# Kernel optimization log

Measured on AMD Instinct MI355X. Metric: run time of the kernel, lower is better.

## Reference

```python
import jax, jax.numpy as jnp
import numpy as np

B, N_ATOM, N_TOK = 1, 1536, 384
C_ATOM, C_PAIR, C_TOK = 128, 16, 384
C_HID, H, L = 32, 4, 3
HID = 2 * C_ATOM  # n_transition = 2
N_QUERY, N_KEY, INF = 32, 128, 1e9


def _ln(x, gamma=None, beta=None, eps=1e-5):
    mu = jnp.mean(x, axis=-1, keepdims=True)
    var = jnp.mean(jnp.square(x - mu), axis=-1, keepdims=True)
    y = (x - mu) * jax.lax.rsqrt(var + eps)
    if gamma is not None:
        y = y * gamma
    if beta is not None:
        y = y + beta
    return y


def _adaln(a, s, gamma_s, Wg, bg, Ws):
    an = _ln(a)            # LN without affine
    sn = _ln(s, gamma_s)   # scale-only LN
    return jax.nn.sigmoid(sn @ Wg + bg) * an + sn @ Ws


def _block_mask():
    # AtomTransformer.forward: 32-query x 128-key block-local mask
    offset = N_QUERY // 2 - 0.5
    n_center = N_ATOM // N_QUERY + 1
    centers = offset + jnp.arange(n_center, dtype=jnp.float32) * N_QUERY
    idx = jnp.arange(N_ATOM, dtype=jnp.float32)[:, None]
    row = (jnp.abs(idx - centers[None, :]) < N_QUERY / 2).astype(jnp.float32)
    col = (jnp.abs(idx - centers[None, :]) < N_KEY / 2).astype(jnp.float32)
    return (row @ col.T - 1.0) * INF   # [N,N]: 0 in-window, -INF outside


def _forward(ref_pos, ref_mask, ref_element, ref_charge, ref_atom_name_chars,
             ref_space_uid, token_mask, atom_to_token_index,
             W_feats, W_ref_offset, W_inv_sq, W_valid, W_l, W_m,
             W_mlp1, W_mlp2, W_mlp3, W_out_tok,
             attn_ada_gamma_s, attn_ada_Wg, attn_ada_bg, attn_ada_Ws,
             Wq, bq, Wk, Wv, lnz_g, lnz_b, Wb, Wgate, Wo, Wsg, bsg,
             tr_ada_gamma_s, tr_ada_Wg, tr_ada_bg, tr_ada_Ws,
             tr_W1, tr_W2, tr_Wog, tr_bog, tr_Wout):
    # --- RefAtomFeatureEmbedder (AF3 Alg 5 lines 1-6) ---
    feats = jnp.concatenate([
        ref_pos, ref_mask[..., None], ref_element, ref_charge[..., None],
        ref_atom_name_chars.reshape(B, N_ATOM, -1), ref_space_uid[..., None]], axis=-1)
    cl = feats @ W_feats                                     # [B,N,C_ATOM]
    d = ref_pos[:, None, :, :] - ref_pos[:, :, None, :]      # d[l,m] = pos[m]-pos[l]
    v = (ref_space_uid[:, None, :] == ref_space_uid[:, :, None]).astype(jnp.float32)[..., None]
    plm = (d @ W_ref_offset) * v
    inv_sq = 1.0 / (1.0 + jnp.sum(d * d, axis=-1, keepdims=True))
    plm = plm + (inv_sq @ W_inv_sq) * v + (v @ W_valid) * v  # [B,N,N,C_PAIR]
    ql = cl
    # --- single -> pair conditioning + pair MLP ---
    crelu = jax.nn.relu(cl)
    plm = plm + (crelu @ W_l)[:, :, None, :] + (crelu @ W_m)[:, None, :, :]
    h = jax.nn.relu(plm) @ W_mlp1
    h = jax.nn.relu(h) @ W_mlp2
    h = jax.nn.relu(h) @ W_mlp3
    plm = plm + h
    # --- AtomTransformer (Alg 7) -> DiffusionTransformer (Alg 23) ---
    beta = _block_mask()                                     # [N,N]
    atom_mask = jnp.einsum('blt,bt->bl', atom_to_token_index, token_mask)
    mask_bias = (atom_mask - 1.0)[:, None, None, :] * INF    # [B,1,1,N]
    a, s = ql, cl
    inv_sqrt = 1.0 / np.sqrt(C_HID)
    for i in range(L):
        # AttentionPairBias (Alg 24)
        an = _adaln(a, s, attn_ada_gamma_s[i], attn_ada_Wg[i], attn_ada_bg[i], attn_ada_Ws[i])
        q = (an @ Wq[i] + bq[i]).reshape(B, N_ATOM, H, C_HID)
        k = (an @ Wk[i]).reshape(B, N_ATOM, H, C_HID)
        vv = (an @ Wv[i]).reshape(B, N_ATOM, H, C_HID)
        zb = _ln(plm, lnz_g[i], lnz_b[i]) @ Wb[i]            # [B,N,N,H]
        logits = (jnp.einsum('bqhc,bkhc->bhqk', q, k) * inv_sqrt
                  + jnp.moveaxis(zb, -1, 1) + beta[None, None] + mask_bias)
        A = jax.nn.softmax(logits, axis=-1)
        o = jnp.einsum('bhqk,bkhc->bqhc', A, vv)
        g = jax.nn.sigmoid(an @ Wgate[i]).reshape(B, N_ATOM, H, C_HID)
        o = (g * o).reshape(B, N_ATOM, H * C_HID) @ Wo[i]
        attn_out = jax.nn.sigmoid(s @ Wsg[i] + bsg[i]) * o
        # ConditionedTransitionBlock (Alg 25) on pre-attention a (Alg 23)
        tn = _adaln(a, s, tr_ada_gamma_s[i], tr_ada_Wg[i], tr_ada_bg[i], tr_ada_Ws[i])
        hh = jax.nn.silu(tn @ tr_W1[i]) * (tn @ tr_W2[i])
        tr_out = jax.nn.sigmoid(s @ tr_Wog[i] + tr_bog[i]) * (hh @ tr_Wout[i])
        a = attn_out + tr_out
    # --- mean-aggregate atoms -> tokens (Alg 5 line 15) ---
    al = jax.nn.relu(a @ W_out_tok)                          # [B,N,C_TOK]
    counts = jnp.maximum(jnp.sum(atom_to_token_index, axis=1), 1.0)
    a_tok = jnp.einsum('blt,blc->btc', atom_to_token_index, al) / counts[..., None]
    return a_tok


def setup_inputs() -> dict:
    key = jax.random.key(0)
    ks = iter(jax.random.split(key, 80))

    def nrm(shape, scale=0.02):
        return jax.random.normal(next(ks), shape, dtype=jnp.float32) * scale

    inp = {}
    inp['ref_pos'] = jax.random.normal(next(ks), (B, N_ATOM, 3), dtype=jnp.float32) * 3.0
    inp['ref_mask'] = jnp.ones((B, N_ATOM), jnp.float32)
    elem = jax.random.randint(next(ks), (B, N_ATOM), 0, 128)
    inp['ref_element'] = jax.nn.one_hot(elem, 128, dtype=jnp.float32)
    inp['ref_charge'] = jax.random.normal(next(ks), (B, N_ATOM), dtype=jnp.float32)
    chars = jax.random.randint(next(ks), (B, N_ATOM, 4), 0, 64)
    inp['ref_atom_name_chars'] = jax.nn.one_hot(chars, 64, dtype=jnp.float32)
    inp['ref_space_uid'] = jnp.broadcast_to(
        (jnp.arange(N_ATOM) // 8).astype(jnp.float32), (B, N_ATOM))
    inp['token_mask'] = jnp.ones((B, N_TOK), jnp.float32)
    tok = (jnp.arange(N_ATOM) * N_TOK) // N_ATOM  # ~4 atoms per token
    inp['atom_to_token_index'] = jnp.broadcast_to(
        jax.nn.one_hot(tok, N_TOK, dtype=jnp.float32), (B, N_ATOM, N_TOK))
    # embedder params
    inp['W_feats'] = nrm((390, C_ATOM))
    inp['W_ref_offset'] = nrm((3, C_PAIR))
    inp['W_inv_sq'] = nrm((1, C_PAIR))
    inp['W_valid'] = nrm((1, C_PAIR))
    inp['W_l'] = nrm((C_ATOM, C_PAIR))
    inp['W_m'] = nrm((C_ATOM, C_PAIR))
    inp['W_mlp1'] = nrm((C_PAIR, C_PAIR))
    inp['W_mlp2'] = nrm((C_PAIR, C_PAIR))
    inp['W_mlp3'] = nrm((C_PAIR, C_PAIR))
    inp['W_out_tok'] = nrm((C_ATOM, C_TOK))
    # DiffusionTransformer params, stacked over L blocks
    inp['attn_ada_gamma_s'] = jnp.ones((L, C_ATOM), jnp.float32)
    inp['attn_ada_Wg'] = nrm((L, C_ATOM, C_ATOM))
    inp['attn_ada_bg'] = jnp.zeros((L, C_ATOM), jnp.float32)
    inp['attn_ada_Ws'] = nrm((L, C_ATOM, C_ATOM))
    inp['Wq'] = nrm((L, C_ATOM, H * C_HID))
    inp['bq'] = jnp.zeros((L, H * C_HID), jnp.float32)
    inp['Wk'] = nrm((L, C_ATOM, H * C_HID))
    inp['Wv'] = nrm((L, C_ATOM, H * C_HID))
    inp['lnz_g'] = jnp.ones((L, C_PAIR), jnp.float32)
    inp['lnz_b'] = jnp.zeros((L, C_PAIR), jnp.float32)
    inp['Wb'] = nrm((L, C_PAIR, H))
    inp['Wgate'] = nrm((L, C_ATOM, H * C_HID))
    inp['Wo'] = nrm((L, H * C_HID, C_ATOM))
    inp['Wsg'] = nrm((L, C_ATOM, C_ATOM))
    inp['bsg'] = jnp.full((L, C_ATOM), -2.0, jnp.float32)
    inp['tr_ada_gamma_s'] = jnp.ones((L, C_ATOM), jnp.float32)
    inp['tr_ada_Wg'] = nrm((L, C_ATOM, C_ATOM))
    inp['tr_ada_bg'] = jnp.zeros((L, C_ATOM), jnp.float32)
    inp['tr_ada_Ws'] = nrm((L, C_ATOM, C_ATOM))
    inp['tr_W1'] = nrm((L, C_ATOM, HID))
    inp['tr_W2'] = nrm((L, C_ATOM, HID))
    inp['tr_Wog'] = nrm((L, C_ATOM, C_ATOM))
    inp['tr_bog'] = jnp.full((L, C_ATOM), -2.0, jnp.float32)
    inp['tr_Wout'] = nrm((L, HID, C_ATOM))
    return inp


def reference(ref_pos, ref_mask, ref_element, ref_charge, ref_atom_name_chars,
              ref_space_uid, token_mask, atom_to_token_index,
              W_feats, W_ref_offset, W_inv_sq, W_valid, W_l, W_m,
              W_mlp1, W_mlp2, W_mlp3, W_out_tok,
              attn_ada_gamma_s, attn_ada_Wg, attn_ada_bg, attn_ada_Ws,
              Wq, bq, Wk, Wv, lnz_g, lnz_b, Wb, Wgate, Wo, Wsg, bsg,
              tr_ada_gamma_s, tr_ada_Wg, tr_ada_bg, tr_ada_Ws,
              tr_W1, tr_W2, tr_Wog, tr_bog, tr_Wout):
    return _forward(ref_pos, ref_mask, ref_element, ref_charge, ref_atom_name_chars,
                    ref_space_uid, token_mask, atom_to_token_index,
                    W_feats, W_ref_offset, W_inv_sq, W_valid, W_l, W_m,
                    W_mlp1, W_mlp2, W_mlp3, W_out_tok,
                    attn_ada_gamma_s, attn_ada_Wg, attn_ada_bg, attn_ada_Ws,
                    Wq, bq, Wk, Wv, lnz_g, lnz_b, Wb, Wgate, Wo, Wsg, bsg,
                    tr_ada_gamma_s, tr_ada_Wg, tr_ada_bg, tr_ada_Ws,
                    tr_W1, tr_W2, tr_Wog, tr_bog, tr_Wout)
```

## Files before the change

kernel.cpp:

```cpp
#include <hip/hip_runtime.h>
#include <math.h>

#define N_ATOM 1536
#define NLAYER 3
#define NC     196608L
#define ZSTRIDE 786432L

struct GD { const float* A; const float* B; float* C; const float* ks; const float* bias;
            const float* sg; const float* ad; int act; int ldb; int ldc; int mode; };
struct GB { GD g[18]; };

__global__ __launch_bounds__(128) void embed_tok_kernel(
    const float* __restrict__ pos, const float* __restrict__ rmask,
    const float* __restrict__ elem, const float* __restrict__ charge,
    const float* __restrict__ chars, const float* __restrict__ uid,
    const float* __restrict__ Wf, const float* __restrict__ W_l, const float* __restrict__ W_m,
    const float* __restrict__ a2t, const float* __restrict__ tmask,
    float* __restrict__ cl, float* __restrict__ aa,
    float* __restrict__ pl, float* __restrict__ pm,
    int* __restrict__ tok, float* __restrict__ amask)
{
  int l = blockIdx.x, c = threadIdx.x;
  __shared__ int sidx[6];
  __shared__ float crow[128];
  if (elem[(long)l * 128 + c] > 0.5f) sidx[0] = c;
  float v0 = chars[(long)l * 256 + c];
  if (v0 > 0.5f) sidx[1 + (c >> 6)] = c & 63;
  float v1 = chars[(long)l * 256 + 128 + c];
  if (v1 > 0.5f) sidx[3 + (c >> 6)] = c & 63;
  for (int j = c; j < 384; j += 128)
    if (a2t[(long)l * 384 + j] > 0.5f) sidx[5] = j;
  __syncthreads();
  float acc = pos[l * 3 + 0] * Wf[c]
            + pos[l * 3 + 1] * Wf[128 + c]
            + pos[l * 3 + 2] * Wf[256 + c]
            + rmask[l] * Wf[384 + c]
            + Wf[(4 + sidx[0]) * 128 + c]
            + charge[l] * Wf[132 * 128 + c]
            + Wf[(133 + sidx[1]) * 128 + c]
            + Wf[(197 + sidx[2]) * 128 + c]
            + Wf[(261 + sidx[3]) * 128 + c]
            + Wf[(325 + sidx[4]) * 128 + c]
            + uid[l] * Wf[389 * 128 + c];
  long gi = (long)l * 128 + c;
  cl[gi] = acc; aa[gi] = acc; crow[c] = fmaxf(acc, 0.f);
  __syncthreads();
  if (c < 32) {
    const float* W = (c < 16) ? W_l : W_m;
    int o = c & 15;
    float s = 0.f;
    for (int cc = 0; cc < 128; cc++) s = fmaf(crow[cc], W[cc * 16 + o], s);
    if (c < 16) pl[l * 16 + o] = s; else pm[l * 16 + o] = s;
  }
  if (c == 127) {
    int j = sidx[5];
    tok[l] = j; amask[l] = tmask[j];
  }
}

__device__ __forceinline__ void gemm64_body(float* sm, const GD d, int row0, int col0) {
  float* As = sm; float* Bs = sm + 2176;
  float* rmu = sm + 4352;
  float* rsd = sm + 4416;
  int tid = threadIdx.x;
  if (d.mode >= 1) {
    int r = tid >> 2, sgi = tid & 3;
    const float* Ar = d.A + (long)(row0 + r) * 128 + sgi * 32;
    float4 vv[8];
    float s1 = 0.f;
#pragma unroll
    for (int c4 = 0; c4 < 8; c4++) {
      vv[c4] = *(const float4*)(Ar + c4 * 4);
      s1 += vv[c4].x + vv[c4].y + vv[c4].z + vv[c4].w;
    }
    s1 += __shfl_xor(s1, 1); s1 += __shfl_xor(s1, 2);
    float mu = s1 * (1.f / 128.f);
    float s2 = 0.f;
#pragma unroll
    for (int c4 = 0; c4 < 8; c4++) {
      float dx = vv[c4].x - mu, dy = vv[c4].y - mu, dz = vv[c4].z - mu, dw = vv[c4].w - mu;
      s2 += dx * dx + dy * dy + dz * dz + dw * dw;
    }
    s2 += __shfl_xor(s2, 1); s2 += __shfl_xor(s2, 2);
    if (sgi == 0) {
      rmu[r] = mu;
      rsd[r] = rsqrtf(s2 * (1.f / 128.f) + 1e-5f);
    }
  }
  int tx = tid & 15, ty = tid >> 4;
  float acc[4][4] = {};
  for (int k0 = 0; k0 < 128; k0 += 32) {
    __syncthreads();
    { int r = tid >> 3, k4 = tid & 7;
#pragma unroll
      for (int half = 0; half < 2; half++) {
        int row = r + half * 32;
        long gro = (long)(row0 + row) * 128 + k0 + k4 * 4;
        float4 v = *(const float4*)(d.A + gro);
        float vals[4] = {v.x, v.y, v.z, v.w};
        if (d.mode >= 1) {
          float mu = rmu[row], sd = rsd[row];
          if (d.mode == 2) {
            float4 sg4 = *(const float4*)(d.sg + gro);
            float4 ad4 = *(const float4*)(d.ad + gro);
            vals[0] = fmaf(sg4.x, (vals[0] - mu) * sd, ad4.x);
            vals[1] = fmaf(sg4.y, (vals[1] - mu) * sd, ad4.y);
            vals[2] = fmaf(sg4.z, (vals[2] - mu) * sd, ad4.z);
            vals[3] = fmaf(sg4.w, (vals[3] - mu) * sd, ad4.w);
          } else {
#pragma unroll
            for (int cc = 0; cc < 4; cc++) vals[cc] = (vals[cc] - mu) * sd;
          }
        }
        if (d.ks) {
          const float* kp = d.ks + k0 + k4 * 4;
#pragma unroll
          for (int cc = 0; cc < 4; cc++) vals[cc] *= kp[cc];
        }
        As[(k4 * 4 + 0) * 68 + row] = vals[0]; As[(k4 * 4 + 1) * 68 + row] = vals[1];
        As[(k4 * 4 + 2) * 68 + row] = vals[2]; As[(k4 * 4 + 3) * 68 + row] = vals[3];
      } }
    { int kk = tid >> 4, n4 = tid & 15;
#pragma unroll
      for (int half = 0; half < 2; half++) {
        int k = kk + half * 16;
        *(float4*)&Bs[k * 68 + n4 * 4] = *(const float4*)(d.B + (long)(k0 + k) * d.ldb + col0 + n4 * 4);
      } }
    __syncthreads();
#pragma unroll
    for (int kk = 0; kk < 32; kk++) {
      float4 a = *(const float4*)&As[kk * 68 + ty * 4];
      float4 b = *(const float4*)&Bs[kk * 68 + tx * 4];
      float av[4] = {a.x, a.y, a.z, a.w}, bv[4] = {b.x, b.y, b.z, b.w};
#pragma unroll
      for (int i = 0; i < 4; i++)
#pragma unroll
        for (int j = 0; j < 4; j++) acc[i][j] = fmaf(av[i], bv[j], acc[i][j]);
    }
  }
  __syncthreads();
#pragma unroll
  for (int i = 0; i < 4; i++) {
    int row = row0 + ty * 4 + i;
#pragma unroll
    for (int j = 0; j < 4; j++) {
      int col = col0 + tx * 4 + j;
      float x = acc[i][j];
      if (d.bias) x += d.bias[col];
      if (d.act == 1) x = 1.f / (1.f + expf(-x));
      else if (d.act == 2) x = fmaxf(x, 0.f);
      d.C[(long)row * d.ldc + col] = x;
    }
  }
}

__global__ __launch_bounds__(256) void gemm64(GB args)
{
  __shared__ float sm[4480];
  gemm64_body(sm, args.g[blockIdx.z], blockIdx.y * 64, blockIdx.x * 64);
}

__global__ __launch_bounds__(256) void zpre_kernel(
    const float* __restrict__ pos, const float* __restrict__ uid,
    const float* __restrict__ Wro, const float* __restrict__ Winv, const float* __restrict__ Wval,
    const float* __restrict__ M1, const float* __restrict__ M2, const float* __restrict__ M3,
    const float* __restrict__ Lg, const float* __restrict__ Lb, const float* __restrict__ Wb,
    const float* __restrict__ pl, const float* __restrict__ pm, float* __restrict__ zb,
    GB ba)
{
  __shared__ float sm[4480];
  int bid = blockIdx.x, tid = threadIdx.x;
  if (bid >= 768) {
    int u = bid - 768;
    GD d = ba.g[u / 48];
    int tt = u % 48;
    gemm64_body(sm, d, (tt >> 1) * 64, (tt & 1) * 64);
    return;
  }
  if (tid < 48)  sm[tid] = Wro[tid];
  if (tid < 16)  { sm[48 + tid] = Winv[tid]; sm[64 + tid] = Wval[tid]; }
  sm[80 + tid] = M1[tid]; sm[336 + tid] = M2[tid]; sm[592 + tid] = M3[tid];
  if (tid < 48)  { sm[848 + tid] = Lg[tid]; sm[896 + tid] = Lb[tid]; }
  if (tid < 192) sm[944 + tid] = Wb[tid];
  __syncthreads();
  const float* sWro = sm;      const float* sWinv = sm + 48;  const float* sWval = sm + 64;
  const float* sM1 = sm + 80;  const float* sM2 = sm + 336;   const float* sM3 = sm + 592;
  const float* sLg = sm + 848; const float* sLb = sm + 896;   const float* sWb = sm + 944;
  int b = bid >> 4;
  int pc = (bid & 15) * 256 + tid;
  int qi = pc >> 7, kj = pc & 127;
  int l = b * 32 + qi, m = b * 32 - 48 + kj;
  long base = (long)(b * 32 + qi) * 128 + kj;
  if (m < 0 || m >= N_ATOM) {
    for (int i = 0; i < NLAYER; i++)
      for (int h = 0; h < 4; h++) zb[i * ZSTRIDE + h * NC + base] = 0.f;
    return;
  }
  float dx = pos[m * 3 + 0] - pos[l * 3 + 0];
  float dy = pos[m * 3 + 1] - pos[l * 3 + 1];
  float dz = pos[m * 3 + 2] - pos[l * 3 + 2];
  float v = (uid[m] == uid[l]) ? 1.f : 0.f;
  float inv = 1.f / (1.f + dx * dx + dy * dy + dz * dz);
  float pv[16], ha[16], hb[16];
#pragma unroll
  for (int j = 0; j < 16; j++)
    pv[j] = v * (dx * sWro[j] + dy * sWro[16 + j] + dz * sWro[32 + j] + inv * sWinv[j] + sWval[j])
            + pl[l * 16 + j] + pm[m * 16 + j];
#pragma unroll
  for (int jo = 0; jo < 16; jo++) { float s = 0.f; for (int ji = 0; ji < 16; ji++) s = fmaf(fmaxf(pv[ji], 0.f), sM1[ji * 16 + jo], s); ha[jo] = s; }
#pragma unroll
  for (int jo = 0; jo < 16; jo++) { float s = 0.f; for (int ji = 0; ji < 16; ji++) s = fmaf(fmaxf(ha[ji], 0.f), sM2[ji * 16 + jo], s); hb[jo] = s; }
#pragma unroll
  for (int jo = 0; jo < 16; jo++) { float s = 0.f; for (int ji = 0; ji < 16; ji++) s = fmaf(fmaxf(hb[ji], 0.f), sM3[ji * 16 + jo], s); ha[jo] = s; }
#pragma unroll
  for (int j = 0; j < 16; j++) pv[j] += ha[j];
  for (int i = 0; i < NLAYER; i++) {
    float mu = 0.f;
#pragma unroll
    for (int j = 0; j < 16; j++) mu += pv[j];
    mu *= (1.f / 16.f);
    float var = 0.f;
#pragma unroll
    for (int j = 0; j < 16; j++) { float dd = pv[j] - mu; var += dd * dd; }
    var *= (1.f / 16.f);
    float rs = rsqrtf(var + 1e-5f);
    float zn[16];
#pragma unroll
    for (int j = 0; j < 16; j++) zn[j] = (pv[j] - mu) * rs * sLg[i * 16 + j] + sLb[i * 16 + j];
    for (int h = 0; h < 4; h++) {
      float s = 0.f;
#pragma unroll
      for (int j = 0; j < 16; j++) s = fmaf(zn[j], sWb[i * 64 + j * 4 + h], s);
      zb[i * ZSTRIDE + h * NC + base] = s;
    }
  }
}

__global__ __launch_bounds__(256) void attn_kernel(
    const float* __restrict__ qb, const float* __restrict__ kb, const float* __restrict__ vb,
    const float* __restrict__ gb, const float* __restrict__ zb, const float* __restrict__ amask,
    float* __restrict__ go)
{
  __shared__ float qs[16][36], ks[128][36], vs[128][36], ps[16][132];
  int bx = blockIdx.x, h = blockIdx.y, t = threadIdx.x;
  int b = bx >> 1, half = bx & 1;
  int q0 = b * 32 + half * 16;
  int kbase = b * 32 - 48;
  const float* zbh = zb + (long)h * NC;
  if (t < 128) {
    int qi = t >> 3, c4 = t & 7;
    *(float4*)&qs[qi][c4 * 4] = *(const float4*)(qb + (long)(q0 + qi) * 128 + h * 32 + c4 * 4);
  }
  for (int idx = t; idx < 128 * 8; idx += 256) {
    int kj = idx >> 3, c4 = idx & 7;
    int m = kbase + kj;
    float4 kv = make_float4(0.f, 0.f, 0.f, 0.f), vv = make_float4(0.f, 0.f, 0.f, 0.f);
    if (m >= 0 && m < N_ATOM) {
      kv = *(const float4*)(kb + (long)m * 128 + h * 32 + c4 * 4);
      vv = *(const float4*)(vb + (long)m * 128 + h * 32 + c4 * 4);
    }
    *(float4*)&ks[kj][c4 * 4] = kv;
    *(float4*)&vs[kj][c4 * 4] = vv;
  }
  __syncthreads();
  const float isq = 0.17677669529663687f;
  for (int p = t; p < 2048; p += 256) {
    int qi = p >> 7, kj = p & 127;
    int m = kbase + kj;
    float s = 0.f;
#pragma unroll
    for (int c4 = 0; c4 < 8; c4++) {
      float4 a = *(const float4*)&qs[qi][c4 * 4];
      float4 k4 = *(const float4*)&ks[kj][c4 * 4];
      s = fmaf(a.x, k4.x, s); s = fmaf(a.y, k4.y, s);
      s = fmaf(a.z, k4.z, s); s = fmaf(a.w, k4.w, s);
    }
    float logit;
    if (m >= 0 && m < N_ATOM) {
      logit = s * isq + zbh[(long)(q0 + qi) * 128 + kj] + (amask[m] - 1.f) * 1e9f;
    } else {
      logit = -1e9f;
    }
    ps[qi][kj] = logit;
  }
  __syncthreads();
  {
    int row = t >> 4, ln = t & 15;
    float mx = -1e30f;
    for (int kj = ln; kj < 128; kj += 16) mx = fmaxf(mx, ps[row][kj]);
#pragma unroll
    for (int o = 8; o > 0; o >>= 1) mx = fmaxf(mx, __shfl_xor(mx, o));
    float sm = 0.f;
    for (int kj = ln; kj < 128; kj += 16) { float e = expf(ps[row][kj] - mx); ps[row][kj] = e; sm += e; }
#pragma unroll
    for (int o = 8; o > 0; o >>= 1) sm += __shfl_xor(sm, o);
    float r = 1.f / sm;
    for (int kj = ln; kj < 128; kj += 16) ps[row][kj] *= r;
  }
  __syncthreads();
  {
    int qi = t >> 4, seg = (t >> 3) & 1, c4 = t & 7;
    float4 acc = make_float4(0.f, 0.f, 0.f, 0.f);
    int kj0 = seg * 64;
#pragma unroll 4
    for (int kj = kj0; kj < kj0 + 64; kj++) {
      float p = ps[qi][kj];
      float4 v = *(const float4*)&vs[kj][c4 * 4];
      acc.x = fmaf(p, v.x, acc.x); acc.y = fmaf(p, v.y, acc.y);
      acc.z = fmaf(p, v.z, acc.z); acc.w = fmaf(p, v.w, acc.w);
    }
    acc.x += __shfl_xor(acc.x, 8);
    acc.y += __shfl_xor(acc.y, 8);
    acc.z += __shfl_xor(acc.z, 8);
    acc.w += __shfl_xor(acc.w, 8);
    if (seg == 0) {
      long gi = (long)(q0 + qi) * 128 + h * 32 + c4 * 4;
      float4 g = *(const float4*)(gb + gi);
      acc.x *= g.x; acc.y *= g.y; acc.z *= g.z; acc.w *= g.w;
      *(float4*)(go + gi) = acc;
    }
  }
}

__global__ __launch_bounds__(256) void gemm_dual32(
    const float* __restrict__ A1, const float* __restrict__ B1,
    const float* __restrict__ h1, const float* __restrict__ h2, const float* __restrict__ B2,
    const float* __restrict__ g1, const float* __restrict__ g2,
    float* __restrict__ C)
{
  __shared__ float As[32 * 36];
  __shared__ float Bs[32 * 68];
  const int N = 128;
  int t = threadIdx.x;
  int row0 = blockIdx.y * 32, col0 = blockIdx.x * 64;
  int tx = t & 15, ty = t >> 4;
  float acc1[2][4] = {}, acc2[2][4] = {};
  for (int k0 = 0; k0 < 128; k0 += 32) {
    __syncthreads();
    { int r = t >> 3, k4 = t & 7;
      float4 v = *(const float4*)(A1 + (long)(row0 + r) * 128 + k0 + k4 * 4);
      As[(k4 * 4 + 0) * 36 + r] = v.x; As[(k4 * 4 + 1) * 36 + r] = v.y;
      As[(k4 * 4 + 2) * 36 + r] = v.z; As[(k4 * 4 + 3) * 36 + r] = v.w;
    }
    for (int e = t; e < 512; e += 256) {
      int k = e >> 4, n4 = e & 15;
      *(float4*)&Bs[k * 68 + n4 * 4] = *(const float4*)(B1 + (long)(k0 + k) * N + col0 + n4 * 4);
    }
    __syncthreads();
#pragma unroll
    for (int kk = 0; kk < 32; kk++) {
      float a0 = As[kk * 36 + ty * 2], a1 = As[kk * 36 + ty * 2 + 1];
      float4 b = *(const float4*)&Bs[kk * 68 + tx * 4];
      float bv[4] = {b.x, b.y, b.z, b.w};
#pragma unroll
      for (int j = 0; j < 4; j++) {
        acc1[0][j] = fmaf(a0, bv[j], acc1[0][j]);
        acc1[1][j] = fmaf(a1, bv[j], acc1[1][j]);
      }
    }
  }
  for (int k0 = 0; k0 < 256; k0 += 32) {
    __syncthreads();
    { int r = t >> 3, k4 = t & 7;
      long o = (long)(row0 + r) * 256 + k0 + k4 * 4;
      float4 x = *(const float4*)(h1 + o);
      float4 y = *(const float4*)(h2 + o);
      As[(k4 * 4 + 0) * 36 + r] = (x.x / (1.f + expf(-x.x))) * y.x;
      As[(k4 * 4 + 1) * 36 + r] = (x.y / (1.f + expf(-x.y))) * y.y;
      As[(k4 * 4 + 2) * 36 + r] = (x.z / (1.f + expf(-x.z))) * y.z;
      As[(k4 * 4 + 3) * 36 + r] = (x.w / (1.f + expf(-x.w))) * y.w;
    }
    for (int e = t; e < 512; e += 256) {
      int k = e >> 4, n4 = e & 15;
      *(float4*)&Bs[k * 68 + n4 * 4] = *(const float4*)(B2 + (long)(k0 + k) * N + col0 + n4 * 4);
    }
    __syncthreads();
#pragma unroll
    for (int kk = 0; kk < 32; kk++) {
      float a0 = As[kk * 36 + ty * 2], a1 = As[kk * 36 + ty * 2 + 1];
      float4 b = *(const float4*)&Bs[kk * 68 + tx * 4];
      float bv[4] = {b.x, b.y, b.z, b.w};
#pragma unroll
      for (int j = 0; j < 4; j++) {
        acc2[0][j] = fmaf(a0, bv[j], acc2[0][j]);
        acc2[1][j] = fmaf(a1, bv[j], acc2[1][j]);
      }
    }
  }
#pragma unroll
  for (int i = 0; i < 2; i++) {
    long o = (long)(row0 + ty * 2 + i) * N + col0 + tx * 4;
    float4 ga = *(const float4*)(g1 + o);
    float4 gb = *(const float4*)(g2 + o);
    float4 r;
    r.x = ga.x * acc1[i][0] + gb.x * acc2[i][0];
    r.y = ga.y * acc1[i][1] + gb.y * acc2[i][1];
    r.z = ga.z * acc1[i][2] + gb.z * acc2[i][2];
    r.w = ga.w * acc1[i][3] + gb.w * acc2[i][3];
    *(float4*)(C + o) = r;
  }
}

__global__ __launch_bounds__(256) void gemm_scatter(
    const float* __restrict__ A, const float* __restrict__ B,
    const int* __restrict__ tok,
    float* __restrict__ out, int K)
{
  __shared__ float As[32][68];
  __shared__ float Bs[32][68];
  int tid = threadIdx.x;
  int row0 = blockIdx.y * 64, col0 = blockIdx.x * 64;
  int tx = tid & 15, ty = tid >> 4;
  float acc[4][4] = {};
  for (int k0 = 0; k0 < K; k0 += 32) {
    __syncthreads();
    { int r = tid >> 3, k4 = tid & 7;
#pragma unroll
      for (int half = 0; half < 2; half++) {
        int row = r + half * 32;
        float4 v = *(const float4*)(A + (long)(row0 + row) * K + k0 + k4 * 4);
        As[k4 * 4 + 0][row] = v.x; As[k4 * 4 + 1][row] = v.y;
        As[k4 * 4 + 2][row] = v.z; As[k4 * 4 + 3][row] = v.w;
      } }
    { int kk = tid >> 4, n4 = tid & 15;
#pragma unroll
      for (int half = 0; half < 2; half++) {
        int k = kk + half * 16;
        float4 v = *(const float4*)(B + (long)(k0 + k) * 384 + col0 + n4 * 4);
        *(float4*)&Bs[k][n4 * 4] = v;
      } }
    __syncthreads();
#pragma unroll
    for (int kk = 0; kk < 32; kk++) {
      float4 a = *(const float4*)&As[kk][ty * 4];
      float4 b = *(const float4*)&Bs[kk][tx * 4];
      float av[4] = {a.x, a.y, a.z, a.w}, bv[4] = {b.x, b.y, b.z, b.w};
#pragma unroll
      for (int i = 0; i < 4; i++)
#pragma unroll
        for (int j = 0; j < 4; j++) acc[i][j] = fmaf(av[i], bv[j], acc[i][j]);
    }
  }
  __syncthreads();
  int r0 = row0 + ty * 4;
  int t0 = tok[r0];
  int cnt = 0;
#pragma unroll
  for (int i = 0; i < 4; i++) cnt += (tok[r0 + i] == t0) ? 1 : 0;
  float inv = 1.f / fmaxf((float)cnt, 1.f);
#pragma unroll
  for (int j = 0; j < 4; j++) {
    int col = col0 + tx * 4 + j;
    float s = 0.f;
#pragma unroll
    for (int i = 0; i < 4; i++)
      if (tok[r0 + i] == t0) s += fmaxf(acc[i][j], 0.f);
    out[(long)t0 * 384 + col] = s * inv;
  }
}

extern "C" void kernel_launch(void* const* d_in, const int* in_sizes, int n_in,
                              void* d_out, int out_size, void* d_ws, size_t ws_size,
                              hipStream_t stream)
{
  const float* pos    = (const float*)d_in[0];
  const float* rmask  = (const float*)d_in[1];
  const float* elem   = (const float*)d_in[2];
  const float* charge = (const float*)d_in[3];
  const float* chars  = (const float*)d_in[4];
  const float* uid    = (const float*)d_in[5];
  const float* tmask  = (const float*)d_in[6];
  const float* a2t    = (const float*)d_in[7];
  const float* Wf     = (const float*)d_in[8];
  const float* Wro    = (const float*)d_in[9];
  const float* Winv   = (const float*)d_in[10];
  const float* Wval   = (const float*)d_in[11];
  const float* W_l    = (const float*)d_in[12];
  const float* W_m    = (const float*)d_in[13];
  const float* M1     = (const float*)d_in[14];
  const float* M2     = (const float*)d_in[15];
  const float* M3     = (const float*)d_in[16];
  const float* Wtok   = (const float*)d_in[17];
  const float* gA     = (const float*)d_in[18];
  const float* WgA    = (const float*)d_in[19];
  const float* bgA    = (const float*)d_in[20];
  const float* WsA    = (const float*)d_in[21];
  const float* Wq     = (const float*)d_in[22];
  const float* bq     = (const float*)d_in[23];
  const float* Wk     = (const float*)d_in[24];
  const float* Wv     = (const float*)d_in[25];
  const float* Lg     = (const float*)d_in[26];
  const float* Lb     = (const float*)d_in[27];
  const float* Wb     = (const float*)d_in[28];
  const float* Wgate  = (const float*)d_in[29];
  const float* Wo     = (const float*)d_in[30];
  const float* Wsg    = (const float*)d_in[31];
  const float* bsg    = (const float*)d_in[32];
  const float* gT     = (const float*)d_in[33];
  const float* WgT    = (const float*)d_in[34];
  const float* bgT    = (const float*)d_in[35];
  const float* WsT    = (const float*)d_in[36];
  const float* trW1   = (const float*)d_in[37];
  const float* trW2   = (const float*)d_in[38];
  const float* Wog    = (const float*)d_in[39];
  const float* bog    = (const float*)d_in[40];
  const float* Wout   = (const float*)d_in[41];
  float* out = (float*)d_out;

  float* ws = (float*)d_ws;
  size_t off = 0;
  auto alloc = [&](size_t n) { float* p = ws + off; off += n; return p; };
  float* cl     = alloc(NC);
  float* aa     = alloc(NC);
  float* qbuf   = alloc(NC);
  float* kbuf   = alloc(NC);
  float* vbuf   = alloc(NC);
  float* gbuf   = alloc(NC);
  float* gobuf  = alloc(NC);
  float* h1     = alloc((size_t)N_ATOM * 256);
  float* h2     = alloc((size_t)N_ATOM * 256);
  float* pl     = alloc((size_t)N_ATOM * 16);
  float* pm     = alloc((size_t)N_ATOM * 16);
  float* zbias  = alloc((size_t)NLAYER * ZSTRIDE);
  float* sgA    = alloc(NC * NLAYER);
  float* adA    = alloc(NC * NLAYER);
  float* sgT    = alloc(NC * NLAYER);
  float* adT    = alloc(NC * NLAYER);
  float* gsg    = alloc(NC * NLAYER);
  float* gog    = alloc(NC * NLAYER);
  float* amask  = alloc(N_ATOM);
  int*   tok    = (int*)alloc(N_ATOM);
  (void)ws_size; (void)in_sizes; (void)n_in; (void)out_size;

  embed_tok_kernel<<<N_ATOM, 128, 0, stream>>>(pos, rmask, elem, charge, chars, uid, Wf,
                                               W_l, W_m, a2t, tmask,
                                               cl, aa, pl, pm, tok, amask);

  {
    GB ba = {};
    for (int i = 0; i < NLAYER; i++) {
      size_t o = (size_t)i * NC;
      ba.g[i * 6 + 0] = { cl, WgA + i * 16384, sgA + o, gA + i * 128, bgA + i * 128, nullptr, nullptr, 1, 128, 128, 1 };
      ba.g[i * 6 + 1] = { cl, WsA + i * 16384, adA + o, gA + i * 128, nullptr,       nullptr, nullptr, 0, 128, 128, 1 };
      ba.g[i * 6 + 2] = { cl, WgT + i * 16384, sgT + o, gT + i * 128, bgT + i * 128, nullptr, nullptr, 1, 128, 128, 1 };
      ba.g[i * 6 + 3] = { cl, WsT + i * 16384, adT + o, gT + i * 128, nullptr,       nullptr, nullptr, 0, 128, 128, 1 };
      ba.g[i * 6 + 4] = { cl, Wsg + i * 16384, gsg + o, nullptr,      bsg + i * 128, nullptr, nullptr, 1, 128, 128, 0 };
      ba.g[i * 6 + 5] = { cl, Wog + i * 16384, gog + o, nullptr,      bog + i * 128, nullptr, nullptr, 1, 128, 128, 0 };
    }
    zpre_kernel<<<768 + 864, 256, 0, stream>>>(pos, uid, Wro, Winv, Wval, M1, M2, M3,
                                               Lg, Lb, Wb, pl, pm, zbias, ba);
  }

  for (int i = 0; i < NLAYER; i++) {
    size_t o = (size_t)i * NC;
    {
      GB ba = {};
      ba.g[0] = { aa, Wq + i * 16384,        qbuf,     nullptr, bq + i * 128, sgA + o, adA + o, 0, 128, 128, 2 };
      ba.g[1] = { aa, Wk + i * 16384,        kbuf,     nullptr, nullptr,      sgA + o, adA + o, 0, 128, 128, 2 };
      ba.g[2] = { aa, Wv + i * 16384,        vbuf,     nullptr, nullptr,      sgA + o, adA + o, 0, 128, 128, 2 };
      ba.g[3] = { aa, Wgate + i * 16384,     gbuf,     nullptr, nullptr,      sgA + o, adA + o, 1, 128, 128, 2 };
      ba.g[4] = { aa, trW1 + i * 32768,       h1,      nullptr, nullptr,      sgT + o, adT + o, 0, 256, 256, 2 };
      ba.g[5] = { aa, trW1 + i * 32768 + 128, h1 + 128, nullptr, nullptr,     sgT + o, adT + o, 0, 256, 256, 2 };
      ba.g[6] = { aa, trW2 + i * 32768,       h2,      nullptr, nullptr,      sgT + o, adT + o, 0, 256, 256, 2 };
      ba.g[7] = { aa, trW2 + i * 32768 + 128, h2 + 128, nullptr, nullptr,     sgT + o, adT + o, 0, 256, 256, 2 };
      gemm64<<<dim3(2, 24, 8), 256, 0, stream>>>(ba);
    }
    attn_kernel<<<dim3(96, 4), 256, 0, stream>>>(qbuf, kbuf, vbuf, gbuf,
                                                 zbias + (size_t)i * ZSTRIDE, amask, gobuf);
    gemm_dual32<<<dim3(2, 48), 256, 0, stream>>>(gobuf, Wo + i * 16384, h1, h2, Wout + i * 32768,
                                                 gsg + o, gog + o, aa);
  }

  gemm_scatter<<<dim3(6, 24), 256, 0, stream>>>(aa, Wtok, tok, out, 128);
}
```

Baseline: 340.1 us.

## Stage full normalized A tile once in LDS and stream B from global

The GEMM body now loads the whole 64x128 A tile once, applies the LayerNorm, modulation and scale in registers while staging it, and writes the full K extent to shared memory behind a single barrier. The four-step K loop with its per-step barriers, the shared-memory B staging, and the second global read of A are removed. B is now read directly from global memory (through cache) inside the inner loop. Shared memory per block roughly doubles, which may reduce occupancy, and uncoalesced B reads per k could add latency.

```diff
diff --git a/kernel.cpp b/kernel.cpp
--- a/kernel.cpp
+++ b/kernel.cpp
@@ -58,87 +58,70 @@
   }
 }
 
-__device__ __forceinline__ void gemm64_body(float* sm, const GD d, int row0, int col0) {
-  float* As = sm; float* Bs = sm + 2176;
-  float* rmu = sm + 4352;
-  float* rsd = sm + 4416;
+__device__ __forceinline__ void gemm64_body(float* As, const GD d, int row0, int col0) {
   int tid = threadIdx.x;
-  if (d.mode >= 1) {
+  {
     int r = tid >> 2, sgi = tid & 3;
-    const float* Ar = d.A + (long)(row0 + r) * 128 + sgi * 32;
+    long rowbase = (long)(row0 + r) * 128 + sgi * 32;
     float4 vv[8];
     float s1 = 0.f;
 #pragma unroll
     for (int c4 = 0; c4 < 8; c4++) {
-      vv[c4] = *(const float4*)(Ar + c4 * 4);
+      vv[c4] = *(const float4*)(d.A + rowbase + c4 * 4);
       s1 += vv[c4].x + vv[c4].y + vv[c4].z + vv[c4].w;
     }
-    s1 += __shfl_xor(s1, 1); s1 += __shfl_xor(s1, 2);
-    float mu = s1 * (1.f / 128.f);
-    float s2 = 0.f;
+    float mu = 0.f, rs = 1.f;
+    if (d.mode >= 1) {
+      s1 += __shfl_xor(s1, 1); s1 += __shfl_xor(s1, 2);
+      mu = s1 * (1.f / 128.f);
+      float s2 = 0.f;
+#pragma unroll
+      for (int c4 = 0; c4 < 8; c4++) {
+        float dx = vv[c4].x - mu, dy = vv[c4].y - mu, dz = vv[c4].z - mu, dw = vv[c4].w - mu;
+        s2 += dx * dx + dy * dy + dz * dz + dw * dw;
+      }
+      s2 += __shfl_xor(s2, 1); s2 += __shfl_xor(s2, 2);
+      rs = rsqrtf(s2 * (1.f / 128.f) + 1e-5f);
+    }
 #pragma unroll
     for (int c4 = 0; c4 < 8; c4++) {
-      float dx = vv[c4].x - mu, dy = vv[c4].y - mu, dz = vv[c4].z - mu, dw = vv[c4].w - mu;
-      s2 += dx * dx + dy * dy + dz * dz + dw * dw;
-    }
-    s2 += __shfl_xor(s2, 1); s2 += __shfl_xor(s2, 2);
-    if (sgi == 0) {
-      rmu[r] = mu;
-      rsd[r] = rsqrtf(s2 * (1.f / 128.f) + 1e-5f);
-    }
-  }
+      float vals[4] = {vv[c4].x, vv[c4].y, vv[c4].z, vv[c4].w};
+      if (d.mode == 2) {
+        float4 sg4 = *(const float4*)(d.sg + rowbase + c4 * 4);
+        float4 ad4 = *(const float4*)(d.ad + rowbase + c4 * 4);
+        vals[0] = fmaf(sg4.x, (vals[0] - mu) * rs, ad4.x);
+        vals[1] = fmaf(sg4.y, (vals[1] - mu) * rs, ad4.y);
+        vals[2] = fmaf(sg4.z, (vals[2] - mu) * rs, ad4.z);
+        vals[3] = fmaf(sg4.w, (vals[3] - mu) * rs, ad4.w);
+      } else if (d.mode == 1) {
+#pragma unroll
+        for (int cc = 0; cc < 4; cc++) vals[cc] = (vals[cc] - mu) * rs;
+      }
+      if (d.ks) {
+        float4 kp = *(const float4*)(d.ks + sgi * 32 + c4 * 4);
+        vals[0] *= kp.x; vals[1] *= kp.y; vals[2] *= kp.z; vals[3] *= kp.w;
+      }
+      int kb = sgi * 32 + c4 * 4;
+      As[(kb + 0) * 68 + r] = vals[0];
+      As[(kb + 1) * 68 + r] = vals[1];
+      As[(kb + 2) * 68 + r] = vals[2];
+      As[(kb + 3) * 68 + r] = vals[3];
+    }
+  }
+  __syncthreads();
   int tx = tid & 15, ty = tid >> 4;
+  const float* Bp = d.B + col0 + tx * 4;
   float acc[4][4] = {};
-  for (int k0 = 0; k0 < 128; k0 += 32) {
-    __syncthreads();
-    { int r = tid >> 3, k4 = tid & 7;
-#pragma unroll
-      for (int half = 0; half < 2; half++) {
-        int row = r + half * 32;
-        long gro = (long)(row0 + row) * 128 + k0 + k4 * 4;
-        float4 v = *(const float4*)(d.A + gro);
-        float vals[4] = {v.x, v.y, v.z, v.w};
-        if (d.mode >= 1) {
-          float mu = rmu[row], sd = rsd[row];
-          if (d.mode == 2) {
-            float4 sg4 = *(const float4*)(d.sg + gro);
-            float4 ad4 = *(const float4*)(d.ad + gro);
-            vals[0] = fmaf(sg4.x, (vals[0] - mu) * sd, ad4.x);
-            vals[1] = fmaf(sg4.y, (vals[1] - mu) * sd, ad4.y);
-            vals[2] = fmaf(sg4.z, (vals[2] - mu) * sd, ad4.z);
-            vals[3] = fmaf(sg4.w, (vals[3] - mu) * sd, ad4.w);
-          } else {
-#pragma unroll
-            for (int cc = 0; cc < 4; cc++) vals[cc] = (vals[cc] - mu) * sd;
-          }
-        }
-        if (d.ks) {
-          const float* kp = d.ks + k0 + k4 * 4;
-#pragma unroll
-          for (int cc = 0; cc < 4; cc++) vals[cc] *= kp[cc];
-        }
-        As[(k4 * 4 + 0) * 68 + row] = vals[0]; As[(k4 * 4 + 1) * 68 + row] = vals[1];
-        As[(k4 * 4 + 2) * 68 + row] = vals[2]; As[(k4 * 4 + 3) * 68 + row] = vals[3];
-      } }
-    { int kk = tid >> 4, n4 = tid & 15;
-#pragma unroll
-      for (int half = 0; half < 2; half++) {
-        int k = kk + half * 16;
-        *(float4*)&Bs[k * 68 + n4 * 4] = *(const float4*)(d.B + (long)(k0 + k) * d.ldb + col0 + n4 * 4);
-      } }
-    __syncthreads();
-#pragma unroll
-    for (int kk = 0; kk < 32; kk++) {
-      float4 a = *(const float4*)&As[kk * 68 + ty * 4];
-      float4 b = *(const float4*)&Bs[kk * 68 + tx * 4];
-      float av[4] = {a.x, a.y, a.z, a.w}, bv[4] = {b.x, b.y, b.z, b.w};
-#pragma unroll
-      for (int i = 0; i < 4; i++)
-#pragma unroll
-        for (int j = 0; j < 4; j++) acc[i][j] = fmaf(av[i], bv[j], acc[i][j]);
-    }
-  }
-  __syncthreads();
+#pragma unroll 8
+  for (int k = 0; k < 128; k++) {
+    float4 b = *(const float4*)(Bp + (long)k * d.ldb);
+    float4 a = *(const float4*)&As[k * 68 + ty * 4];
+    float av[4] = {a.x, a.y, a.z, a.w}, bv[4] = {b.x, b.y, b.z, b.w};
+#pragma unroll
+    for (int i = 0; i < 4; i++)
+#pragma unroll
+      for (int j = 0; j < 4; j++) acc[i][j] = fmaf(av[i], bv[j], acc[i][j]);
+  }
 #pragma unroll
   for (int i = 0; i < 4; i++) {
     int row = row0 + ty * 4 + i;
@@ -156,7 +139,7 @@
 
 __global__ __launch_bounds__(256) void gemm64(GB args)
 {
-  __shared__ float sm[4480];
+  __shared__ float sm[8704];
   gemm64_body(sm, args.g[blockIdx.z], blockIdx.y * 64, blockIdx.x * 64);
 }
 
@@ -168,7 +151,7 @@
     const float* __restrict__ pl, const float* __restrict__ pm, float* __restrict__ zb,
     GB ba)
 {
-  __shared__ float sm[4480];
+  __shared__ float sm[8704];
   int bid = blockIdx.x, tid = threadIdx.x;
   if (bid >= 768) {
     int u = bid - 768;
```

After: 352.4 us. +3.6%, slower.

## Move transition output GEMM into attention launch as extra blocks

Applied to the files above, without the earlier changes.

The SwiGLU transition down-projection (K=256) moves out of the post-attention dual GEMM and runs as 96 extra blocks appended to the attention kernel launch, writing a gated partial result to a new buffer. The remaining Wo kernel only does the K=128 attention output projection and adds the precomputed transition term. The aim is to fill idle CUs during attention (384 blocks) and shorten the serial tail kernel. This costs an extra buffer write and read, and the larger shared-memory union may lower occupancy for the attention blocks.

```diff
diff --git a/kernel.cpp b/kernel.cpp
--- a/kernel.cpp
+++ b/kernel.cpp
@@ -156,7 +156,7 @@
 
 __global__ __launch_bounds__(256) void gemm64(GB args)
 {
-  __shared__ float sm[4480];
+  __shared__ __align__(16) float sm[4480];
   gemm64_body(sm, args.g[blockIdx.z], blockIdx.y * 64, blockIdx.x * 64);
 }
 
@@ -168,7 +168,7 @@
     const float* __restrict__ pl, const float* __restrict__ pm, float* __restrict__ zb,
     GB ba)
 {
-  __shared__ float sm[4480];
+  __shared__ __align__(16) float sm[4480];
   int bid = blockIdx.x, tid = threadIdx.x;
   if (bid >= 768) {
     int u = bid - 768;
@@ -236,20 +236,72 @@
   }
 }
 
-__global__ __launch_bounds__(256) void attn_kernel(
+__global__ __launch_bounds__(256) void attn_tr_kernel(
     const float* __restrict__ qb, const float* __restrict__ kb, const float* __restrict__ vb,
     const float* __restrict__ gb, const float* __restrict__ zb, const float* __restrict__ amask,
-    float* __restrict__ go)
-{
-  __shared__ float qs[16][36], ks[128][36], vs[128][36], ps[16][132];
-  int bx = blockIdx.x, h = blockIdx.y, t = threadIdx.x;
+    float* __restrict__ go,
+    const float* __restrict__ h1, const float* __restrict__ h2, const float* __restrict__ B2,
+    const float* __restrict__ g2, float* __restrict__ trbuf)
+{
+  __shared__ __align__(16) float sm[11904];
+  int bid = blockIdx.x, t = threadIdx.x;
+  if (bid >= 384) {
+    int u = bid - 384;
+    int row0 = (u >> 1) * 32, col0 = (u & 1) * 64;
+    float* As = sm; float* Bs = sm + 1152;
+    int tx = t & 15, ty = t >> 4;
+    float acc2[2][4] = {};
+    for (int k0 = 0; k0 < 256; k0 += 32) {
+      __syncthreads();
+      { int r = t >> 3, k4 = t & 7;
+        long o = (long)(row0 + r) * 256 + k0 + k4 * 4;
+        float4 x = *(const float4*)(h1 + o);
+        float4 y = *(const float4*)(h2 + o);
+        As[(k4 * 4 + 0) * 36 + r] = (x.x / (1.f + expf(-x.x))) * y.x;
+        As[(k4 * 4 + 1) * 36 + r] = (x.y / (1.f + expf(-x.y))) * y.y;
+        As[(k4 * 4 + 2) * 36 + r] = (x.z / (1.f + expf(-x.z))) * y.z;
+        As[(k4 * 4 + 3) * 36 + r] = (x.w / (1.f + expf(-x.w))) * y.w;
+      }
+      for (int e = t; e < 512; e += 256) {
+        int k = e >> 4, n4 = e & 15;
+        *(float4*)&Bs[k * 68 + n4 * 4] = *(const float4*)(B2 + (long)(k0 + k) * 128 + col0 + n4 * 4);
+      }
+      __syncthreads();
+#pragma unroll
+      for (int kk = 0; kk < 32; kk++) {
+        float a0 = As[kk * 36 + ty * 2], a1 = As[kk * 36 + ty * 2 + 1];
+        float4 b = *(const float4*)&Bs[kk * 68 + tx * 4];
+        float bv[4] = {b.x, b.y, b.z, b.w};
+#pragma unroll
+        for (int j = 0; j < 4; j++) {
+          acc2[0][j] = fmaf(a0, bv[j], acc2[0][j]);
+          acc2[1][j] = fmaf(a1, bv[j], acc2[1][j]);
+        }
+      }
+    }
+#pragma unroll
+    for (int i = 0; i < 2; i++) {
+      long o = (long)(row0 + ty * 2 + i) * 128 + col0 + tx * 4;
+      float4 g4 = *(const float4*)(g2 + o);
+      float4 r;
+      r.x = g4.x * acc2[i][0]; r.y = g4.y * acc2[i][1];
+      r.z = g4.z * acc2[i][2]; r.w = g4.w * acc2[i][3];
+      *(float4*)(trbuf + o) = r;
+    }
+    return;
+  }
+  float* qs = sm;
+  float* ks = sm + 576;
+  float* vs = sm + 5184;
+  float* ps = sm + 9792;
+  int h = bid / 96, bx = bid - h * 96;
   int b = bx >> 1, half = bx & 1;
   int q0 = b * 32 + half * 16;
   int kbase = b * 32 - 48;
   const float* zbh = zb + (long)h * NC;
   if (t < 128) {
     int qi = t >> 3, c4 = t & 7;
-    *(float4*)&qs[qi][c4 * 4] = *(const float4*)(qb + (long)(q0 + qi) * 128 + h * 32 + c4 * 4);
+    *(float4*)&qs[qi * 36 + c4 * 4] = *(const float4*)(qb + (long)(q0 + qi) * 128 + h * 32 + c4 * 4);
   }
   for (int idx = t; idx < 128 * 8; idx += 256) {
     int kj = idx >> 3, c4 = idx & 7;
@@ -259,8 +311,8 @@
       kv = *(const float4*)(kb + (long)m * 128 + h * 32 + c4 * 4);
       vv = *(const float4*)(vb + (long)m * 128 + h * 32 + c4 * 4);
     }
-    *(float4*)&ks[kj][c4 * 4] = kv;
-    *(float4*)&vs[kj][c4 * 4] = vv;
+    *(float4*)&ks[kj * 36 + c4 * 4] = kv;
+    *(float4*)&vs[kj * 36 + c4 * 4] = vv;
   }
   __syncthreads();
   const float isq = 0.17677669529663687f;
@@ -270,8 +322,8 @@
     float s = 0.f;
 #pragma unroll
     for (int c4 = 0; c4 < 8; c4++) {
-      float4 a = *(const float4*)&qs[qi][c4 * 4];
-      float4 k4 = *(const float4*)&ks[kj][c4 * 4];
+      float4 a = *(const float4*)&qs[qi * 36 + c4 * 4];
+      float4 k4 = *(const float4*)&ks[kj * 36 + c4 * 4];
       s = fmaf(a.x, k4.x, s); s = fmaf(a.y, k4.y, s);
       s = fmaf(a.z, k4.z, s); s = fmaf(a.w, k4.w, s);
     }
@@ -281,21 +333,21 @@
     } else {
       logit = -1e9f;
     }
-    ps[qi][kj] = logit;
+    ps[qi * 132 + kj] = logit;
   }
   __syncthreads();
   {
     int row = t >> 4, ln = t & 15;
     float mx = -1e30f;
-    for (int kj = ln; kj < 128; kj += 16) mx = fmaxf(mx, ps[row][kj]);
+    for (int kj = ln; kj < 128; kj += 16) mx = fmaxf(mx, ps[row * 132 + kj]);
 #pragma unroll
     for (int o = 8; o > 0; o >>= 1) mx = fmaxf(mx, __shfl_xor(mx, o));
-    float sm = 0.f;
-    for (int kj = ln; kj < 128; kj += 16) { float e = expf(ps[row][kj] - mx); ps[row][kj] = e; sm += e; }
-#pragma unroll
-    for (int o = 8; o > 0; o >>= 1) sm += __shfl_xor(sm, o);
-    float r = 1.f / sm;
-    for (int kj = ln; kj < 128; kj += 16) ps[row][kj] *= r;
+    float smv = 0.f;
+    for (int kj = ln; kj < 128; kj += 16) { float e = expf(ps[row * 132 + kj] - mx); ps[row * 132 + kj] = e; smv += e; }
+#pragma unroll
+    for (int o = 8; o > 0; o >>= 1) smv += __shfl_xor(smv, o);
+    float r = 1.f / smv;
+    for (int kj = ln; kj < 128; kj += 16) ps[row * 132 + kj] *= r;
   }
   __syncthreads();
   {
@@ -304,8 +356,8 @@
     int kj0 = seg * 64;
 #pragma unroll 4
     for (int kj = kj0; kj < kj0 + 64; kj++) {
-      float p = ps[qi][kj];
-      float4 v = *(const float4*)&vs[kj][c4 * 4];
+      float p = ps[qi * 132 + kj];
+      float4 v = *(const float4*)&vs[kj * 36 + c4 * 4];
       acc.x = fmaf(p, v.x, acc.x); acc.y = fmaf(p, v.y, acc.y);
       acc.z = fmaf(p, v.z, acc.z); acc.w = fmaf(p, v.w, acc.w);
     }
@@ -322,19 +374,18 @@
   }
 }
 
-__global__ __launch_bounds__(256) void gemm_dual32(
+__global__ __launch_bounds__(256) void wo_kernel(
     const float* __restrict__ A1, const float* __restrict__ B1,
-    const float* __restrict__ h1, const float* __restrict__ h2, const float* __restrict__ B2,
-    const float* __restrict__ g1, const float* __restrict__ g2,
+    const float* __restrict__ g1, const float* __restrict__ tr,
     float* __restrict__ C)
 {
-  __shared__ float As[32 * 36];
-  __shared__ float Bs[32 * 68];
+  __shared__ __align__(16) float As[32 * 36];
+  __shared__ __align__(16) float Bs[32 * 68];
   const int N = 128;
   int t = threadIdx.x;
   int row0 = blockIdx.y * 32, col0 = blockIdx.x * 64;
   int tx = t & 15, ty = t >> 4;
-  float acc1[2][4] = {}, acc2[2][4] = {};
+  float acc1[2][4] = {};
   for (int k0 = 0; k0 < 128; k0 += 32) {
     __syncthreads();
     { int r = t >> 3, k4 = t & 7;
@@ -359,44 +410,16 @@
       }
     }
   }
-  for (int k0 = 0; k0 < 256; k0 += 32) {
-    __syncthreads();
-    { int r = t >> 3, k4 = t & 7;
-      long o = (long)(row0 + r) * 256 + k0 + k4 * 4;
-      float4 x = *(const float4*)(h1 + o);
-      float4 y = *(const float4*)(h2 + o);
-      As[(k4 * 4 + 0) * 36 + r] = (x.x / (1.f + expf(-x.x))) * y.x;
-      As[(k4 * 4 + 1) * 36 + r] = (x.y / (1.f + expf(-x.y))) * y.y;
-      As[(k4 * 4 + 2) * 36 + r] = (x.z / (1.f + expf(-x.z))) * y.z;
-      As[(k4 * 4 + 3) * 36 + r] = (x.w / (1.f + expf(-x.w))) * y.w;
-    }
-    for (int e = t; e < 512; e += 256) {
-      int k = e >> 4, n4 = e & 15;
-      *(float4*)&Bs[k * 68 + n4 * 4] = *(const float4*)(B2 + (long)(k0 + k) * N + col0 + n4 * 4);
-    }
-    __syncthreads();
-#pragma unroll
-    for (int kk = 0; kk < 32; kk++) {
-      float a0 = As[kk * 36 + ty * 2], a1 = As[kk * 36 + ty * 2 + 1];
-      float4 b = *(const float4*)&Bs[kk * 68 + tx * 4];
-      float bv[4] = {b.x, b.y, b.z, b.w};
-#pragma unroll
-      for (int j = 0; j < 4; j++) {
-        acc2[0][j] = fmaf(a0, bv[j], acc2[0][j]);
-        acc2[1][j] = fmaf(a1, bv[j], acc2[1][j]);
-      }
-    }
-  }
 #pragma unroll
   for (int i = 0; i < 2; i++) {
     long o = (long)(row0 + ty * 2 + i) * N + col0 + tx * 4;
     float4 ga = *(const float4*)(g1 + o);
-    float4 gb = *(const float4*)(g2 + o);
+    float4 tv = *(const float4*)(tr + o);
     float4 r;
-    r.x = ga.x * acc1[i][0] + gb.x * acc2[i][0];
-    r.y = ga.y * acc1[i][1] + gb.y * acc2[i][1];
-    r.z = ga.z * acc1[i][2] + gb.z * acc2[i][2];
-    r.w = ga.w * acc1[i][3] + gb.w * acc2[i][3];
+    r.x = ga.x * acc1[i][0] + tv.x;
+    r.y = ga.y * acc1[i][1] + tv.y;
+    r.z = ga.z * acc1[i][2] + tv.z;
+    r.w = ga.w * acc1[i][3] + tv.w;
     *(float4*)(C + o) = r;
   }
 }
@@ -406,8 +429,8 @@
     const int* __restrict__ tok,
     float* __restrict__ out, int K)
 {
-  __shared__ float As[32][68];
-  __shared__ float Bs[32][68];
+  __shared__ __align__(16) float As[32][68];
+  __shared__ __align__(16) float Bs[32][68];
   int tid = threadIdx.x;
   int row0 = blockIdx.y * 64, col0 = blockIdx.x * 64;
   int tx = tid & 15, ty = tid >> 4;
@@ -517,6 +540,7 @@
   float* vbuf   = alloc(NC);
   float* gbuf   = alloc(NC);
   float* gobuf  = alloc(NC);
+  float* trbuf  = alloc(NC);
   float* h1     = alloc((size_t)N_ATOM * 256);
   float* h2     = alloc((size_t)N_ATOM * 256);
   float* pl     = alloc((size_t)N_ATOM * 16);
@@ -565,10 +589,10 @@
       ba.g[7] = { aa, trW2 + i * 32768 + 128, h2 + 128, nullptr, nullptr,     sgT + o, adT + o, 0, 256, 256, 2 };
       gemm64<<<dim3(2, 24, 8), 256, 0, stream>>>(ba);
     }
-    attn_kernel<<<dim3(96, 4), 256, 0, stream>>>(qbuf, kbuf, vbuf, gbuf,
-                                                 zbias + (size_t)i * ZSTRIDE, amask, gobuf);
-    gemm_dual32<<<dim3(2, 48), 256, 0, stream>>>(gobuf, Wo + i * 16384, h1, h2, Wout + i * 32768,
-                                                 gsg + o, gog + o, aa);
+    attn_tr_kernel<<<480, 256, 0, stream>>>(qbuf, kbuf, vbuf, gbuf,
+                                            zbias + (size_t)i * ZSTRIDE, amask, gobuf,
+                                            h1, h2, Wout + i * 32768, gog + o, trbuf);
+    wo_kernel<<<dim3(2, 48), 256, 0, stream>>>(gobuf, Wo + i * 16384, gsg + o, trbuf, aa);
   }
 
   gemm_scatter<<<dim3(6, 24), 256, 0, stream>>>(aa, Wtok, tok, out, 128);
```

Result: faster. 326.3 us (-4.1%).
